# Kernel optimization log

Measured on AMD Instinct MI355X. Metric: run time of the kernel, lower is better.

## Reference

```python
import jax, jax.numpy as jnp
import numpy as np

C = 256
NUM_HEADS = 4
REDUCTION = 4
RED = C // REDUCTION           # 64
HEAD_DIM = RED // NUM_HEADS    # 16
SCALE = HEAD_DIM ** -0.5
LN_EPS = 1e-5


def setup_inputs() -> dict:
    key = jax.random.key(0)
    ks = jax.random.split(key, 9)
    B, H, W = 2, 64, 64
    x = jax.random.normal(ks[0], (B, C, H, W), dtype=jnp.float32)
    # LayerNorm params
    norm_w = jnp.ones((C,), jnp.float32)
    norm_b = jnp.zeros((C,), jnp.float32)
    # Linear weights (torch layout: [out, in]), y = x @ W.T
    qkv_w = jax.random.normal(ks[1], (3 * RED, C), jnp.float32) * (C ** -0.5)
    out_w = jax.random.normal(ks[2], (C, RED), jnp.float32) * (RED ** -0.5)
    # 1x1 conv weights, stored as [out_c, in_c]
    conv1_w = jax.random.normal(ks[3], (C // 2, C), jnp.float32) * (C ** -0.5)
    conv1_b = jax.random.normal(ks[4], (C // 2,), jnp.float32) * 0.01
    conv2_w = jax.random.normal(ks[5], (1, C // 2), jnp.float32) * ((C // 2) ** -0.5)
    conv2_b = jax.random.normal(ks[6], (1,), jnp.float32) * 0.01
    gamma = jnp.ones((1,), jnp.float32) * 0.5  # nonzero so output depends on attention
    return {"x": x, "norm_w": norm_w, "norm_b": norm_b, "qkv_w": qkv_w,
            "out_w": out_w, "conv1_w": conv1_w, "conv1_b": conv1_b,
            "conv2_w": conv2_w, "conv2_b": conv2_b, "gamma": gamma}


def reference(x, norm_w, norm_b, qkv_w, out_w, conv1_w, conv1_b, conv2_w, conv2_b, gamma):
    B, C_, H, W = x.shape
    N = H * W
    # [B, N, C]
    xf = x.reshape(B, C_, N).transpose(0, 2, 1)
    # LayerNorm over channel dim
    mu = jnp.mean(xf, axis=-1, keepdims=True)
    var = jnp.mean(jnp.square(xf - mu), axis=-1, keepdims=True)
    xn = (xf - mu) * jax.lax.rsqrt(var + LN_EPS) * norm_w + norm_b
    # QKV projection -> [B, N, 3*RED]
    qkv = jnp.einsum('bnc,oc->bno', xn, qkv_w)
    q, k, v = jnp.split(qkv, 3, axis=-1)
    def heads(t):  # [B, N, RED] -> [B, h, N, d]
        return t.reshape(B, N, NUM_HEADS, HEAD_DIM).transpose(0, 2, 1, 3)
    q, k, v = heads(q), heads(k), heads(v)
    attn = jax.nn.softmax(jnp.einsum('bhnd,bhmd->bhnm', q, k) * SCALE, axis=-1)
    # dynamic weight branch: two 1x1 convs on raw x
    d1 = jax.nn.relu(jnp.einsum('oc,bchw->bohw', conv1_w, x) + conv1_b[None, :, None, None])
    dyn = (jnp.einsum('oc,bchw->bohw', conv2_w, d1) + conv2_b[None, :, None, None])  # [B,1,H,W]
    dyn = dyn.reshape(B, 1, N)  # broadcast over heads
    # per-query row scaling of attention
    attn = attn * dyn[:, :, :, None]
    out = jnp.einsum('bhnm,bhmd->bhnd', attn, v)            # [B,h,N,d]
    out = out.transpose(0, 2, 1, 3).reshape(B, N, RED)      # [B,N,RED]
    out = jnp.einsum('bnr,cr->bnc', out, out_w)             # [B,N,C]
    out = out.transpose(0, 2, 1).reshape(B, C_, H, W)
    return jax.nn.sigmoid(gamma[0] * out + x)
```

## Files before the change

### kernel.cpp

```cpp
#include <hip/hip_runtime.h>
#include <cstdint>
#include <cstddef>

#define LOG2E 1.44269504088896340736f

typedef float  f32x16 __attribute__((ext_vector_type(16)));
typedef __bf16 bf16x8 __attribute__((ext_vector_type(8)));

union BF8 { bf16x8 v; uint u[4]; ushort us[8]; };

__device__ __forceinline__ uint pack_bf(float a, float b) {
    uint ua = __float_as_uint(a) + 0x8000u;
    uint ub = __float_as_uint(b) + 0x8000u;
    return __builtin_amdgcn_perm(ub, ua, 0x07060302u);
}
__device__ __forceinline__ float bf_lo(uint u) { return __uint_as_float(u << 16); }
__device__ __forceinline__ float bf_hi(uint u) { return __uint_as_float(u & 0xFFFF0000u); }

__global__ __launch_bounds__(256) void convert_w_kernel(
    const float* __restrict__ qkv_w, const float* __restrict__ c1w,
    const float* __restrict__ out_w,
    ushort* __restrict__ qkvw_b, ushort* __restrict__ c1w_b, ushort* __restrict__ ow_b)
{
    const int g = (blockIdx.x * 256 + threadIdx.x) * 4;
    const float* src; ushort* dst; int off; float sc = 1.f;
    if (g < 49152)      { src = qkv_w; dst = qkvw_b; off = g;
                          if (g < 16384) sc = 0.25f * LOG2E; }
    else if (g < 81920) { src = c1w;   dst = c1w_b;  off = g - 49152; }
    else                { src = out_w; dst = ow_b;   off = g - 81920; }
    float4 v = *(const float4*)(src + off);
    uint2 pk;
    pk.x = pack_bf(v.x * sc, v.y * sc);
    pk.y = pack_bf(v.z * sc, v.w * sc);
    *(uint2*)(dst + off) = pk;
}

__global__ __launch_bounds__(256) void ln_cast_kernel(
    const float* __restrict__ x, const float* __restrict__ nw, const float* __restrict__ nb,
    ushort* __restrict__ xnb, ushort* __restrict__ xrb)
{
    __shared__ uint  xp[32 * 144];
    __shared__ float red1[256], red2[256];
    __shared__ float muS[32], rsS[32];

    const int t  = threadIdx.x;
    const int b  = blockIdx.x >> 7;
    const int n0 = (blockIdx.x & 127) * 32;
    const int j  = t & 31;
    const int cg = t >> 5;
    const size_t xb = (size_t)b * 256 * 4096 + n0 + j;

    float v[32];
    #pragma unroll
    for (int i = 0; i < 32; ++i) v[i] = x[xb + (size_t)(cg * 32 + i) * 4096];
    float s1 = 0.f, s2 = 0.f;
    #pragma unroll
    for (int i = 0; i < 32; ++i) { s1 += v[i]; s2 += v[i] * v[i]; }
    #pragma unroll
    for (int i = 0; i < 16; ++i)
        xp[j * 144 + cg * 16 + i] = pack_bf(v[2 * i], v[2 * i + 1]);
    red1[t] = s1; red2[t] = s2;
    __syncthreads();
    if (t < 32) {
        float a = 0.f, q = 0.f;
        #pragma unroll
        for (int g2 = 0; g2 < 8; ++g2) { a += red1[g2 * 32 + t]; q += red2[g2 * 32 + t]; }
        float mu  = a * (1.f / 256.f);
        float var = q * (1.f / 256.f) - mu * mu;
        muS[t] = mu; rsS[t] = rsqrtf(fmaxf(var, 0.f) + 1e-5f);
    }
    __syncthreads();

    for (int it = 0; it < 4; ++it) {
        int lin = it * 256 + t;
        int px = lin >> 5, q = lin & 31;
        uint4 raw = *(uint4*)&xp[px * 144 + q * 4];
        size_t row = (size_t)blockIdx.x * 32 + px;
        *(uint4*)(xrb + row * 256 + q * 8) = raw;

        float mu = muS[px], rs = rsS[px];
        const float4 w0 = *(const float4*)(nw + q * 8);
        const float4 w1 = *(const float4*)(nw + q * 8 + 4);
        const float4 b0 = *(const float4*)(nb + q * 8);
        const float4 b1 = *(const float4*)(nb + q * 8 + 4);
        float e0 = (bf_lo(raw.x) - mu) * rs * w0.x + b0.x;
        float e1 = (bf_hi(raw.x) - mu) * rs * w0.y + b0.y;
        float e2 = (bf_lo(raw.y) - mu) * rs * w0.z + b0.z;
        float e3 = (bf_hi(raw.y) - mu) * rs * w0.w + b0.w;
        float e4 = (bf_lo(raw.z) - mu) * rs * w1.x + b1.x;
        float e5 = (bf_hi(raw.z) - mu) * rs * w1.y + b1.y;
        float e6 = (bf_lo(raw.w) - mu) * rs * w1.z + b1.z;
        float e7 = (bf_hi(raw.w) - mu) * rs * w1.w + b1.w;
        uint4 o;
        o.x = pack_bf(e0, e1); o.y = pack_bf(e2, e3);
        o.z = pack_bf(e4, e5); o.w = pack_bf(e6, e7);
        *(uint4*)(xnb + row * 256 + q * 8) = o;
    }
}

__global__ __launch_bounds__(256) void qkvconv_kernel(
    const ushort* __restrict__ xnb, const ushort* __restrict__ xrb,
    const ushort* __restrict__ qkvw_b, const ushort* __restrict__ c1w_b,
    const float* __restrict__ c1b, const float* __restrict__ c2w,
    const float* __restrict__ c2b,
    ushort* __restrict__ Qb, ushort* __restrict__ Kb, ushort* __restrict__ Vsw,
    float* __restrict__ dynb)
{
    __shared__ float trans[4][32 * 33];
    const int t    = threadIdx.x;
    const int w    = t >> 6;
    const int lane = t & 63;
    const int m    = lane & 31;
    const int h    = lane >> 5;
    const int pg   = blockIdx.x;
    const int b    = pg >> 7;
    const int n0   = (pg & 127) * 32;
    float* tr = trans[w];

    if (w < 3) {
        const ushort* bp  = xnb + ((size_t)pg * 32 + m) * 256 + h * 8;
        const ushort* ap0 = qkvw_b + ((size_t)(w * 64 + m)) * 256 + h * 8;
        const ushort* ap1 = ap0 + 32 * 256;
        f32x16 acc0, acc1;
        #pragma unroll
        for (int i = 0; i < 16; ++i) { acc0[i] = 0.f; acc1[i] = 0.f; }
        #pragma unroll 4
        for (int ks = 0; ks < 16; ++ks) {
            bf16x8 bf = *(const bf16x8*)(bp  + ks * 16);
            bf16x8 a0 = *(const bf16x8*)(ap0 + ks * 16);
            bf16x8 a1 = *(const bf16x8*)(ap1 + ks * 16);
            acc0 = __builtin_amdgcn_mfma_f32_32x32x16_bf16(a0, bf, acc0, 0, 0, 0);
            acc1 = __builtin_amdgcn_mfma_f32_32x32x16_bf16(a1, bf, acc1, 0, 0, 0);
        }
        for (int ti = 0; ti < 2; ++ti) {
            const f32x16& A = ti ? acc1 : acc0;
            #pragma unroll
            for (int r = 0; r < 16; ++r)
                tr[((r & 3) + 8 * (r >> 2) + 4 * h) * 33 + m] = A[r];
            if (w < 2) {
                ushort* dst = (w == 0) ? Qb : Kb;
                #pragma unroll
                for (int it = 0; it < 2; ++it) {
                    int unit = it * 2 + h;
                    int hl = unit >> 1, half = unit & 1;
                    float v0 = tr[(hl * 16 + half * 8 + 0) * 33 + m];
                    float v1 = tr[(hl * 16 + half * 8 + 1) * 33 + m];
                    float v2 = tr[(hl * 16 + half * 8 + 2) * 33 + m];
                    float v3 = tr[(hl * 16 + half * 8 + 3) * 33 + m];
                    float v4 = tr[(hl * 16 + half * 8 + 4) * 33 + m];
                    float v5 = tr[(hl * 16 + half * 8 + 5) * 33 + m];
                    float v6 = tr[(hl * 16 + half * 8 + 6) * 33 + m];
                    float v7 = tr[(hl * 16 + half * 8 + 7) * 33 + m];
                    uint4 pk;
                    pk.x = pack_bf(v0, v1); pk.y = pack_bf(v2, v3);
                    pk.z = pack_bf(v4, v5); pk.w = pack_bf(v6, v7);
                    int head = ti * 2 + hl;
                    *(uint4*)(dst + ((size_t)(b * 4 + head) * 4096 + n0 + m) * 16 + half * 8) = pk;
                }
            } else {
                int d = lane & 15, u = lane >> 4;
                #pragma unroll
                for (int it = 0; it < 4; ++it) {
                    int unit = it * 4 + u;
                    int hl = unit >> 3, sg = unit & 7;
                    float v0 = tr[(hl * 16 + d) * 33 + sg * 4 + 0];
                    float v1 = tr[(hl * 16 + d) * 33 + sg * 4 + 1];
                    float v2 = tr[(hl * 16 + d) * 33 + sg * 4 + 2];
                    float v3 = tr[(hl * 16 + d) * 33 + sg * 4 + 3];
                    uint2 pk; pk.x = pack_bf(v0, v1); pk.y = pack_bf(v2, v3);
                    int head = ti * 2 + hl;
                    *(uint2*)(Vsw + (((size_t)(b * 4 + head) * 1024 + (pg & 127) * 8 + sg) * 16 + d) * 4) = pk;
                }
            }
        }
    } else {
        const ushort* bp = xrb + ((size_t)pg * 32 + m) * 256 + h * 8;
        f32x16 acc[4];
        #pragma unroll
        for (int ti = 0; ti < 4; ++ti)
            #pragma unroll
            for (int i = 0; i < 16; ++i) acc[ti][i] = 0.f;
        #pragma unroll 2
        for (int ks = 0; ks < 16; ++ks) {
            bf16x8 bf = *(const bf16x8*)(bp + ks * 16);
            #pragma unroll
            for (int ti = 0; ti < 4; ++ti) {
                bf16x8 a = *(const bf16x8*)(c1w_b + ((size_t)(ti * 32 + m)) * 256 + ks * 16 + h * 8);
                acc[ti] = __builtin_amdgcn_mfma_f32_32x32x16_bf16(a, bf, acc[ti], 0, 0, 0);
            }
        }
        float partial = 0.f;
        for (int ti = 0; ti < 4; ++ti) {
            #pragma unroll
            for (int r = 0; r < 16; ++r)
                tr[((r & 3) + 8 * (r >> 2) + 4 * h) * 33 + m] = acc[ti][r];
            #pragma unroll
            for (int i = 0; i < 16; ++i) {
                int og = ti * 32 + h * 16 + i;
                partial += fmaxf(tr[(h * 16 + i) * 33 + m] + c1b[og], 0.f) * c2w[og];
            }
        }
        float tot = partial + __shfl_xor(partial, 32);
        if (lane < 32) dynb[(size_t)b * 4096 + n0 + m] = c2b[0] + tot;
    }
}

__global__ __launch_bounds__(256) void attn_kernel(
    const ushort* __restrict__ Qb, const ushort* __restrict__ Kb,
    const ushort* __restrict__ Vsw, float* __restrict__ AO2)
{
    const int t   = threadIdx.x;
    const int lid = t & 63;
    const int w   = t >> 6;
    const int c   = lid & 31;
    const int h   = lid >> 5;

    const int bi = blockIdx.x;
    const int kb = bi & 1;
    const int qb = (bi >> 1) & 31;
    const int bh = bi >> 6;
    const int nq = qb * 128 + w * 32;

    const bf16x8 qf = *(const bf16x8*)(Qb + ((size_t)bh * 4096 + nq + c) * 16 + h * 8);

    f32x16 oacc, zf;
    #pragma unroll
    for (int i = 0; i < 16; ++i) { oacc[i] = 0.f; zf[i] = 0.f; }

    const ushort* kp = Kb + ((size_t)bh * 4096 + kb * 2048 + c) * 16 + h * 8;
    const ushort* vb = Vsw + (size_t)bh * 65536 + ((size_t)kb * 512 + h) * 64 + c * 4;

    #pragma unroll 2
    for (int ch = 0; ch < 64; ++ch) {
        const bf16x8 kf = *(const bf16x8*)kp;
        f32x16 s = __builtin_amdgcn_mfma_f32_32x32x16_bf16(kf, qf, zf, 0, 0, 0);

        BF8 p1, p2;
        #pragma unroll
        for (int jj = 0; jj < 4; ++jj) {
            p1.u[jj] = pack_bf(__builtin_amdgcn_exp2f(s[2*jj]),   __builtin_amdgcn_exp2f(s[2*jj+1]));
            p2.u[jj] = pack_bf(__builtin_amdgcn_exp2f(s[8+2*jj]), __builtin_amdgcn_exp2f(s[8+2*jj+1]));
        }

        BF8 a1, a2;
        if (c < 16) {
            const uint2 g1 = *(const uint2*)(vb);
            const uint2 g2 = *(const uint2*)(vb + 128);
            const uint2 g3 = *(const uint2*)(vb + 256);
            const uint2 g4 = *(const uint2*)(vb + 384);
            a1.u[0] = g1.x; a1.u[1] = g1.y; a1.u[2] = g2.x; a1.u[3] = g2.y;
            a2.u[0] = g3.x; a2.u[1] = g3.y; a2.u[2] = g4.x; a2.u[3] = g4.y;
        } else {
            const uint f = (c == 16) ? 0x3F803F80u : 0u;
            a1.u[0] = a1.u[1] = a1.u[2] = a1.u[3] = f;
            a2.u[0] = a2.u[1] = a2.u[2] = a2.u[3] = f;
        }

        oacc = __builtin_amdgcn_mfma_f32_32x32x16_bf16(a1.v, p1.v, oacc, 0, 0, 0);
        oacc = __builtin_amdgcn_mfma_f32_32x32x16_bf16(a2.v, p2.v, oacc, 0, 0, 0);

        kp += 512; vb += 512;
    }

    float* ao = AO2 + ((size_t)(kb * 8 + bh) * 4096 + nq + c) * 20;
    float4 s0; s0.x = oacc[0]; s0.y = oacc[1]; s0.z = oacc[2]; s0.w = oacc[3];
    float4 s1; s1.x = oacc[4]; s1.y = oacc[5]; s1.z = oacc[6]; s1.w = oacc[7];
    *(float4*)(ao + 4 * h)     = s0;
    *(float4*)(ao + 8 + 4 * h) = s1;
    if (h == 0) ao[16] = oacc[8];
}

__global__ __launch_bounds__(256) void final_kernel(
    const float* __restrict__ AO2, const float* __restrict__ dynb,
    const ushort* __restrict__ ow_b, const float* __restrict__ x,
    const float* __restrict__ gamma, float* __restrict__ out)
{
    __shared__ float trans[4][32 * 33];
    const int t    = threadIdx.x;
    const int w    = t >> 6;
    const int lane = t & 63;
    const int m    = lane & 31;
    const int h    = lane >> 5;
    const int pg   = blockIdx.x;
    const int b    = pg >> 7;
    const int n0   = (pg & 127) * 32;
    float* tr = trans[w];

    const float dyn_px = dynb[(size_t)b * 4096 + n0 + m];
    const ushort* a0p = ow_b + ((size_t)(w * 64 + m)) * 64 + h * 8;
    const ushort* a1p = a0p + 32 * 64;

    f32x16 acc0, acc1;
    #pragma unroll
    for (int i = 0; i < 16; ++i) { acc0[i] = 0.f; acc1[i] = 0.f; }

    #pragma unroll
    for (int ks = 0; ks < 4; ++ks) {
        const float* r0 = AO2 + ((size_t)(b * 4 + ks) * 4096 + n0 + m) * 20;
        const float* r1 = r0 + (size_t)8 * 4096 * 20;
        float l   = r0[16] + r1[16];
        float fac = dyn_px / l;
        float4 u0 = *(const float4*)(r0 + h * 8);
        float4 u1 = *(const float4*)(r0 + h * 8 + 4);
        float4 t0 = *(const float4*)(r1 + h * 8);
        float4 t1 = *(const float4*)(r1 + h * 8 + 4);
        float e0 = (u0.x + t0.x) * fac, e1 = (u0.y + t0.y) * fac;
        float e2 = (u0.z + t0.z) * fac, e3 = (u0.w + t0.w) * fac;
        float e4 = (u1.x + t1.x) * fac, e5 = (u1.y + t1.y) * fac;
        float e6 = (u1.z + t1.z) * fac, e7 = (u1.w + t1.w) * fac;
        BF8 bfr;
        bfr.u[0] = pack_bf(e0, e1); bfr.u[1] = pack_bf(e2, e3);
        bfr.u[2] = pack_bf(e4, e5); bfr.u[3] = pack_bf(e6, e7);
        bf16x8 af0 = *(const bf16x8*)(a0p + ks * 16);
        bf16x8 af1 = *(const bf16x8*)(a1p + ks * 16);
        acc0 = __builtin_amdgcn_mfma_f32_32x32x16_bf16(af0, bfr.v, acc0, 0, 0, 0);
        acc1 = __builtin_amdgcn_mfma_f32_32x32x16_bf16(af1, bfr.v, acc1, 0, 0, 0);
    }

    const float g = gamma[0];
    for (int ti = 0; ti < 2; ++ti) {
        const f32x16& A = ti ? acc1 : acc0;
        #pragma unroll
        for (int r = 0; r < 16; ++r)
            tr[((r & 3) + 8 * (r >> 2) + 4 * h) * 33 + m] = A[r];
        int ob = w * 64 + ti * 32;
        #pragma unroll 4
        for (int it = 0; it < 16; ++it) {
            int o = it * 2 + h;
            float vv = tr[o * 33 + m];
            size_t idx = ((size_t)b * 256 + ob + o) * 4096 + n0 + m;
            float z = g * vv + x[idx];
            out[idx] = 1.f / (1.f + __builtin_amdgcn_exp2f(-z * LOG2E));
        }
    }
}

extern "C" void kernel_launch(void* const* d_in, const int* in_sizes, int n_in,
                              void* d_out, int out_size, void* d_ws, size_t ws_size,
                              hipStream_t stream)
{
    const float* x      = (const float*)d_in[0];
    const float* norm_w = (const float*)d_in[1];
    const float* norm_b = (const float*)d_in[2];
    const float* qkv_w  = (const float*)d_in[3];
    const float* out_w  = (const float*)d_in[4];
    const float* c1w    = (const float*)d_in[5];
    const float* c1b    = (const float*)d_in[6];
    const float* c2w    = (const float*)d_in[7];
    const float* c2b    = (const float*)d_in[8];
    const float* gamma  = (const float*)d_in[9];

    char* ws = (char*)d_ws;
    ushort* Qb     = (ushort*)ws;
    ushort* Kb     = Qb + 524288;
    ushort* Vsw    = Kb + 524288;
    ushort* qkvw_b = Vsw + 524288;
    ushort* c1w_b  = qkvw_b + 49152;
    ushort* ow_b   = c1w_b + 32768;
    float*  dynb   = (float*)(ws + 3342336);
    ushort* xnb    = (ushort*)(ws + 3375104);
    ushort* xrb    = xnb + 2097152;
    float*  AO2    = (float*)(ws + 3375104);

    hipLaunchKernelGGL(convert_w_kernel, dim3(96), dim3(256), 0, stream,
                       qkv_w, c1w, out_w, qkvw_b, c1w_b, ow_b);
    hipLaunchKernelGGL(ln_cast_kernel, dim3(256), dim3(256), 0, stream,
                       x, norm_w, norm_b, xnb, xrb);
    hipLaunchKernelGGL(qkvconv_kernel, dim3(256), dim3(256), 0, stream,
                       xnb, xrb, qkvw_b, c1w_b, c1b, c2w, c2b, Qb, Kb, Vsw, dynb);
    hipLaunchKernelGGL(attn_kernel, dim3(512), dim3(256), 0, stream,
                       Qb, Kb, Vsw, AO2);
    hipLaunchKernelGGL(final_kernel, dim3(256), dim3(256), 0, stream,
                       AO2, dynb, ow_b, x, gamma, (float*)d_out);
}
```

Measured before the change: 139.5 us.

## Fuse LayerNorm/cast kernel into QKV+conv projection kernel via shared memory

Merges the LayerNorm-and-bf16-cast kernel into the QKV/conv1 MFMA kernel, so the normalized and raw bf16 activations are staged in LDS instead of written to and reread from global workspace. This drops one kernel launch and a round trip of about 4 MB of intermediate traffic. The LDS layout is rearranged to feed the MFMA B operand directly, and LDS use per block goes up, which may lower occupancy. LayerNorm is now applied to the fp32 values rather than to bf16-rounded ones.

```diff
diff --git a/kernel.cpp b/kernel.cpp
--- a/kernel.cpp
+++ b/kernel.cpp
@@ -35,90 +35,87 @@
     *(uint2*)(dst + off) = pk;
 }
 
-__global__ __launch_bounds__(256) void ln_cast_kernel(
+__global__ __launch_bounds__(256) void lnqkv_kernel(
     const float* __restrict__ x, const float* __restrict__ nw, const float* __restrict__ nb,
-    ushort* __restrict__ xnb, ushort* __restrict__ xrb)
-{
-    __shared__ uint  xp[32 * 144];
-    __shared__ float red1[256], red2[256];
-    __shared__ float muS[32], rsS[32];
-
-    const int t  = threadIdx.x;
-    const int b  = blockIdx.x >> 7;
-    const int n0 = (blockIdx.x & 127) * 32;
-    const int j  = t & 31;
-    const int cg = t >> 5;
-    const size_t xb = (size_t)b * 256 * 4096 + n0 + j;
-
-    float v[32];
-    #pragma unroll
-    for (int i = 0; i < 32; ++i) v[i] = x[xb + (size_t)(cg * 32 + i) * 4096];
-    float s1 = 0.f, s2 = 0.f;
-    #pragma unroll
-    for (int i = 0; i < 32; ++i) { s1 += v[i]; s2 += v[i] * v[i]; }
-    #pragma unroll
-    for (int i = 0; i < 16; ++i)
-        xp[j * 144 + cg * 16 + i] = pack_bf(v[2 * i], v[2 * i + 1]);
-    red1[t] = s1; red2[t] = s2;
-    __syncthreads();
-    if (t < 32) {
-        float a = 0.f, q = 0.f;
-        #pragma unroll
-        for (int g2 = 0; g2 < 8; ++g2) { a += red1[g2 * 32 + t]; q += red2[g2 * 32 + t]; }
-        float mu  = a * (1.f / 256.f);
-        float var = q * (1.f / 256.f) - mu * mu;
-        muS[t] = mu; rsS[t] = rsqrtf(fmaxf(var, 0.f) + 1e-5f);
-    }
-    __syncthreads();
-
-    for (int it = 0; it < 4; ++it) {
-        int lin = it * 256 + t;
-        int px = lin >> 5, q = lin & 31;
-        uint4 raw = *(uint4*)&xp[px * 144 + q * 4];
-        size_t row = (size_t)blockIdx.x * 32 + px;
-        *(uint4*)(xrb + row * 256 + q * 8) = raw;
-
-        float mu = muS[px], rs = rsS[px];
-        const float4 w0 = *(const float4*)(nw + q * 8);
-        const float4 w1 = *(const float4*)(nw + q * 8 + 4);
-        const float4 b0 = *(const float4*)(nb + q * 8);
-        const float4 b1 = *(const float4*)(nb + q * 8 + 4);
-        float e0 = (bf_lo(raw.x) - mu) * rs * w0.x + b0.x;
-        float e1 = (bf_hi(raw.x) - mu) * rs * w0.y + b0.y;
-        float e2 = (bf_lo(raw.y) - mu) * rs * w0.z + b0.z;
-        float e3 = (bf_hi(raw.y) - mu) * rs * w0.w + b0.w;
-        float e4 = (bf_lo(raw.z) - mu) * rs * w1.x + b1.x;
-        float e5 = (bf_hi(raw.z) - mu) * rs * w1.y + b1.y;
-        float e6 = (bf_lo(raw.w) - mu) * rs * w1.z + b1.z;
-        float e7 = (bf_hi(raw.w) - mu) * rs * w1.w + b1.w;
-        uint4 o;
-        o.x = pack_bf(e0, e1); o.y = pack_bf(e2, e3);
-        o.z = pack_bf(e4, e5); o.w = pack_bf(e6, e7);
-        *(uint4*)(xnb + row * 256 + q * 8) = o;
-    }
-}
-
-__global__ __launch_bounds__(256) void qkvconv_kernel(
-    const ushort* __restrict__ xnb, const ushort* __restrict__ xrb,
     const ushort* __restrict__ qkvw_b, const ushort* __restrict__ c1w_b,
     const float* __restrict__ c1b, const float* __restrict__ c2w,
     const float* __restrict__ c2b,
     ushort* __restrict__ Qb, ushort* __restrict__ Kb, ushort* __restrict__ Vsw,
     float* __restrict__ dynb)
 {
+    __shared__ uint  XN[32 * 32 * 4];
+    __shared__ uint  XR[32 * 32 * 4];
     __shared__ float trans[4][32 * 33];
+    __shared__ float red1[256], red2[256];
+    __shared__ float muS[32], rsS[32];
+
     const int t    = threadIdx.x;
+    const int pg   = blockIdx.x;
+    const int b    = pg >> 7;
+    const int n0   = (pg & 127) * 32;
+
+    {
+        const int j  = t & 31;
+        const int cg = t >> 5;
+        const size_t xb = (size_t)b * 256 * 4096 + n0 + j;
+        float v[32];
+        #pragma unroll
+        for (int i = 0; i < 32; ++i) v[i] = x[xb + (size_t)(cg * 32 + i) * 4096];
+        float s1 = 0.f, s2 = 0.f;
+        #pragma unroll
+        for (int i = 0; i < 32; ++i) { s1 += v[i]; s2 += v[i] * v[i]; }
+        #pragma unroll
+        for (int kk = 0; kk < 4; ++kk) {
+            uint4 pk;
+            pk.x = pack_bf(v[kk * 8 + 0], v[kk * 8 + 1]);
+            pk.y = pack_bf(v[kk * 8 + 2], v[kk * 8 + 3]);
+            pk.z = pack_bf(v[kk * 8 + 4], v[kk * 8 + 5]);
+            pk.w = pack_bf(v[kk * 8 + 6], v[kk * 8 + 7]);
+            *(uint4*)&XR[((cg * 4 + kk) * 32 + j) * 4] = pk;
+        }
+        red1[t] = s1; red2[t] = s2;
+        __syncthreads();
+        if (t < 32) {
+            float a = 0.f, q = 0.f;
+            #pragma unroll
+            for (int g2 = 0; g2 < 8; ++g2) { a += red1[g2 * 32 + t]; q += red2[g2 * 32 + t]; }
+            float mu  = a * (1.f / 256.f);
+            float var = q * (1.f / 256.f) - mu * mu;
+            muS[t] = mu; rsS[t] = rsqrtf(fmaxf(var, 0.f) + 1e-5f);
+        }
+        __syncthreads();
+        const float mu = muS[j], rs = rsS[j];
+        #pragma unroll
+        for (int kk = 0; kk < 4; ++kk) {
+            const float4 w0 = *(const float4*)(nw + cg * 32 + kk * 8);
+            const float4 w1 = *(const float4*)(nw + cg * 32 + kk * 8 + 4);
+            const float4 b0 = *(const float4*)(nb + cg * 32 + kk * 8);
+            const float4 b1 = *(const float4*)(nb + cg * 32 + kk * 8 + 4);
+            float e0 = (v[kk * 8 + 0] - mu) * rs * w0.x + b0.x;
+            float e1 = (v[kk * 8 + 1] - mu) * rs * w0.y + b0.y;
+            float e2 = (v[kk * 8 + 2] - mu) * rs * w0.z + b0.z;
+            float e3 = (v[kk * 8 + 3] - mu) * rs * w0.w + b0.w;
+            float e4 = (v[kk * 8 + 4] - mu) * rs * w1.x + b1.x;
+            float e5 = (v[kk * 8 + 5] - mu) * rs * w1.y + b1.y;
+            float e6 = (v[kk * 8 + 6] - mu) * rs * w1.z + b1.z;
+            float e7 = (v[kk * 8 + 7] - mu) * rs * w1.w + b1.w;
+            uint4 o;
+            o.x = pack_bf(e0, e1); o.y = pack_bf(e2, e3);
+            o.z = pack_bf(e4, e5); o.w = pack_bf(e6, e7);
+            *(uint4*)&XN[((cg * 4 + kk) * 32 + j) * 4] = o;
+        }
+    }
+    __syncthreads();
+
     const int w    = t >> 6;
     const int lane = t & 63;
     const int m    = lane & 31;
     const int h    = lane >> 5;
-    const int pg   = blockIdx.x;
-    const int b    = pg >> 7;
-    const int n0   = (pg & 127) * 32;
     float* tr = trans[w];
+    const ushort* xnB = (const ushort*)XN;
+    const ushort* xrB = (const ushort*)XR;
 
     if (w < 3) {
-        const ushort* bp  = xnb + ((size_t)pg * 32 + m) * 256 + h * 8;
         const ushort* ap0 = qkvw_b + ((size_t)(w * 64 + m)) * 256 + h * 8;
         const ushort* ap1 = ap0 + 32 * 256;
         f32x16 acc0, acc1;
@@ -126,7 +123,7 @@
         for (int i = 0; i < 16; ++i) { acc0[i] = 0.f; acc1[i] = 0.f; }
         #pragma unroll 4
         for (int ks = 0; ks < 16; ++ks) {
-            bf16x8 bf = *(const bf16x8*)(bp  + ks * 16);
+            bf16x8 bf = *(const bf16x8*)(xnB + ((ks * 2 + h) * 32 + m) * 8);
             bf16x8 a0 = *(const bf16x8*)(ap0 + ks * 16);
             bf16x8 a1 = *(const bf16x8*)(ap1 + ks * 16);
             acc0 = __builtin_amdgcn_mfma_f32_32x32x16_bf16(a0, bf, acc0, 0, 0, 0);
@@ -174,7 +171,6 @@
             }
         }
     } else {
-        const ushort* bp = xrb + ((size_t)pg * 32 + m) * 256 + h * 8;
         f32x16 acc[4];
         #pragma unroll
         for (int ti = 0; ti < 4; ++ti)
@@ -182,7 +178,7 @@
             for (int i = 0; i < 16; ++i) acc[ti][i] = 0.f;
         #pragma unroll 2
         for (int ks = 0; ks < 16; ++ks) {
-            bf16x8 bf = *(const bf16x8*)(bp + ks * 16);
+            bf16x8 bf = *(const bf16x8*)(xrB + ((ks * 2 + h) * 32 + m) * 8);
             #pragma unroll
             for (int ti = 0; ti < 4; ++ti) {
                 bf16x8 a = *(const bf16x8*)(c1w_b + ((size_t)(ti * 32 + m)) * 256 + ks * 16 + h * 8);
@@ -358,16 +354,13 @@
     ushort* c1w_b  = qkvw_b + 49152;
     ushort* ow_b   = c1w_b + 32768;
     float*  dynb   = (float*)(ws + 3342336);
-    ushort* xnb    = (ushort*)(ws + 3375104);
-    ushort* xrb    = xnb + 2097152;
     float*  AO2    = (float*)(ws + 3375104);
 
     hipLaunchKernelGGL(convert_w_kernel, dim3(96), dim3(256), 0, stream,
                        qkv_w, c1w, out_w, qkvw_b, c1w_b, ow_b);
-    hipLaunchKernelGGL(ln_cast_kernel, dim3(256), dim3(256), 0, stream,
-                       x, norm_w, norm_b, xnb, xrb);
-    hipLaunchKernelGGL(qkvconv_kernel, dim3(256), dim3(256), 0, stream,
-                       xnb, xrb, qkvw_b, c1w_b, c1b, c2w, c2b, Qb, Kb, Vsw, dynb);
+    hipLaunchKernelGGL(lnqkv_kernel, dim3(256), dim3(256), 0, stream,
+                       x, norm_w, norm_b, qkvw_b, c1w_b, c1b, c2w, c2b,
+                       Qb, Kb, Vsw, dynb);
     hipLaunchKernelGGL(attn_kernel, dim3(512), dim3(256), 0, stream,
                        Qb, Kb, Vsw, AO2);
     hipLaunchKernelGGL(final_kernel, dim3(256), dim3(256), 0, stream,
```

After: 133.7 us. 1.04x faster.
